# Kernel tuning notes

Hardware: AMD Instinct MI355X
Metric: run time of the kernel (lower is better)

The kernel has to match this reference:

```python
import jax, jax.numpy as jnp
import numpy as np

EPS = 1e-5

def _conv(x, w, groups=1):
    # x: NCHW, w: OIHW, VALID padding, stride 1
    return jax.lax.conv_general_dilated(
        x, w, window_strides=(1, 1), padding='VALID',
        feature_group_count=groups,
        dimension_numbers=('NCHW', 'OIHW', 'NCHW'))

def _bn(x, gamma, beta, mean, var):
    # eval-mode BatchNorm2d over channel dim
    inv = jax.lax.rsqrt(var + EPS) * gamma
    return x * inv[None, :, None, None] + (beta - mean * inv)[None, :, None, None]

def _xcorr_depthwise(x, kernel):
    # per-sample depthwise cross-correlation via grouped conv
    B, C, H, W = x.shape
    xr = x.reshape(1, B * C, H, W)
    kr = kernel.reshape(B * C, 1, kernel.shape[2], kernel.shape[3])
    out = _conv(xr, kr, groups=B * C)  # [1, B*C, Ho, Wo]
    return out.reshape(B, C, out.shape[2], out.shape[3])

def setup_inputs() -> dict:
    key = jax.random.key(0)
    ks = jax.random.split(key, 16)
    B, Cin, H, Oc = 128, 256, 256, 256
    inp = {
        'kernel': jax.random.normal(ks[0], (B, Cin, 7, 7), jnp.float32),
        'search': jax.random.normal(ks[1], (B, Cin, 31, 31), jnp.float32),
        # conv_kernel tower
        'wk': jax.random.normal(ks[2], (H, Cin, 3, 3), jnp.float32) * 0.05,
        'gk': jax.random.normal(ks[3], (H,), jnp.float32) * 0.1 + 1.0,
        'bk': jax.random.normal(ks[4], (H,), jnp.float32) * 0.1,
        'mk': jax.random.normal(ks[5], (H,), jnp.float32) * 0.1,
        'vk': jax.random.uniform(ks[6], (H,), jnp.float32) + 0.5,
        # conv_search tower
        'ws': jax.random.normal(ks[7], (H, Cin, 3, 3), jnp.float32) * 0.05,
        'gs': jax.random.normal(ks[8], (H,), jnp.float32) * 0.1 + 1.0,
        'bs': jax.random.normal(ks[9], (H,), jnp.float32) * 0.1,
        'ms': jax.random.normal(ks[10], (H,), jnp.float32) * 0.1,
        'vs': jax.random.uniform(ks[11], (H,), jnp.float32) + 0.5,
        # head: 1x1 conv -> BN -> ReLU -> 1x1 conv (with bias)
        'wh1': jax.random.normal(ks[12], (H, H, 1, 1), jnp.float32) * 0.05,
        'gh': jax.random.normal(ks[13], (H,), jnp.float32) * 0.1 + 1.0,
        'bh': jax.random.normal(ks[14], (H,), jnp.float32) * 0.1,
        'mh': jnp.zeros((H,), jnp.float32),
        'vh': jnp.ones((H,), jnp.float32),
        'wh2': jax.random.normal(ks[15], (Oc, H, 1, 1), jnp.float32) * 0.05,
        'bh2': jnp.zeros((Oc,), jnp.float32),
    }
    return inp

def reference(kernel, search, wk, gk, bk, mk, vk, ws, gs, bs, ms, vs,
              wh1, gh, bh, mh, vh, wh2, bh2):
    k = jax.nn.relu(_bn(_conv(kernel, wk), gk, bk, mk, vk))   # [B,H,5,5]
    s = jax.nn.relu(_bn(_conv(search, ws), gs, bs, ms, vs))   # [B,H,29,29]
    feat = _xcorr_depthwise(s, k)                              # [B,H,25,25]
    h = jax.nn.relu(_bn(_conv(feat, wh1), gh, bh, mh, vh))
    out = _conv(h, wh2) + bh2[None, :, None, None]            # [B,Oc,25,25]
    return out
```

## Files before the change

### kernel.cpp

```cpp
#include <hip/hip_runtime.h>
#include <hip/hip_bf16.h>
#include <cstdint>
#include <cstddef>

typedef unsigned short u16;
typedef __attribute__((ext_vector_type(8))) __bf16 bf16x8;
typedef __attribute__((ext_vector_type(4))) float f32x4;

#define EPS_BN 1e-5f

__device__ __forceinline__ u16 f2bf(float f) {
    union { float f; uint32_t u; } v; v.f = f;
    uint32_t u = v.u;
    u += 0x7FFFu + ((u >> 16) & 1u);
    return (u16)(u >> 16);
}
__device__ __forceinline__ float bf2f(u16 s) {
    union { uint32_t u; float f; } v; v.u = ((uint32_t)s) << 16;
    return v.f;
}

union Pack8 { u16 u[8]; uint4 v4; };
union Pack4 { u16 u[4]; uint2 v2; };

typedef __attribute__((address_space(1))) const unsigned char as1c;
typedef __attribute__((address_space(3))) unsigned char as3;
__device__ __forceinline__ void gld_lds16(const void* g, void* l) {
    __builtin_amdgcn_global_load_lds((as1c*)g, (as3*)l, 16, 0, 0);
}

__device__ __forceinline__ void tr_tile(const float* __restrict__ in,
                                        u16* __restrict__ out,
                                        int P, int b, int p0)
{
    const int cp = threadIdx.x & 31;
    const int pr = threadIdx.x >> 5;
    const float* ib = in + (size_t)b * 256 * P + (size_t)cp * 8 * P;
    u16* ob = out + (size_t)(b * P + p0) * 256 + cp * 8;

    #pragma unroll
    for (int it = 0; it < 8; it++) {
        int px = it * 8 + pr;
        int p  = p0 + px;
        bool ok = (p < P);
        int pc = ok ? p : (P - 1);
        Pack8 pk;
        #pragma unroll
        for (int i = 0; i < 8; i++)
            pk.u[i] = f2bf(ib[(size_t)i * P + pc]);
        if (ok) *(uint4*)(ob + (size_t)px * 256) = pk.v4;
    }
}

__global__ __launch_bounds__(256)
void tr_all(const float* __restrict__ s, const float* __restrict__ k,
            u16* __restrict__ so, u16* __restrict__ ko)
{
    int blk = blockIdx.x;
    if (blk < 2048) {
        tr_tile(s, so, 961, blk >> 4, (blk & 15) * 64);
    } else {
        tr_tile(k, ko, 49, blk - 2048, 0);
    }
}

template<int TAPS, bool NHWC_OUT, typename OutT, bool RELU>
__global__ __launch_bounds__(256)
void conv_gemm(const u16* __restrict__ in, const u16* __restrict__ W,
               const float* __restrict__ scale, const float* __restrict__ shift,
               OutT* __restrict__ out, int Hi, int Wi, int Ho, int Wo)
{
    constexpr int KT = TAPS * 256;
    constexpr int KB = KT / 64;
    const int HoWo = Ho * Wo;

    __shared__ u16 Alds[8192];
    __shared__ u16 Blds[8192];

    const int tid = threadIdx.x;
    const int it = blockIdx.x;
    const int jt = blockIdx.y;
    const int wv = tid >> 6;
    const int lane = tid & 63;

    const int c8 = tid & 7;
    const int t3 = tid >> 3;
    const int csw = c8 ^ (t3 & 7);

    const u16* gA[4];
    const u16* gB[4];
    #pragma unroll
    for (int q = 0; q < 4; q++) {
        int r = q * 32 + t3;
        gA[q] = W + (size_t)(it * 128 + r) * KT + csw * 8;
        int jg = jt * 128 + r;
        int bb = jg / HoWo;
        int msp = jg - bb * HoWo;
        int oyp = msp / Wo;
        int oxp = msp - oyp * Wo;
        gB[q] = in + ((size_t)(bb * Hi + oyp) * Wi + oxp) * 256 + csw * 8;
    }

    const int wi = (wv >> 1) * 64;
    const int wj = (wv & 1) * 64;
    const int lr = lane & 15;
    const int lq = lane >> 4;

    f32x4 acc[4][4];
    #pragma unroll
    for (int a = 0; a < 4; a++)
        #pragma unroll
        for (int b = 0; b < 4; b++)
            acc[a][b] = (f32x4){0.f, 0.f, 0.f, 0.f};

    for (int kb = 0; kb < KB; kb++) {
        const int tap = (TAPS == 1) ? 0 : (kb >> 2);
        const int c0  = (TAPS == 1) ? (kb * 64) : ((kb & 3) * 64);
        int ky = 0, kx = 0;
        if (TAPS == 9) { ky = tap / 3; kx = tap - ky * 3; }
        const int aoff = tap * 256 + c0;
        const int boff = (ky * Wi + kx) * 256 + c0;
        __syncthreads();
        #pragma unroll
        for (int q = 0; q < 4; q++)
            gld_lds16(gA[q] + aoff, Alds + q * 2048 + wv * 512);
        #pragma unroll
        for (int q = 0; q < 4; q++)
            gld_lds16(gB[q] + boff, Blds + q * 2048 + wv * 512);
        __syncthreads();
        #pragma unroll
        for (int ks = 0; ks < 2; ks++) {
            bf16x8 af[4], bfr[4];
            const int ck = ks * 4 + lq;
            #pragma unroll
            for (int f = 0; f < 4; f++) {
                int ra = wi + f * 16 + lr;
                af[f]  = *(const bf16x8*)&Alds[ra * 64 + ((ck ^ (ra & 7)) * 8)];
                int rb = wj + f * 16 + lr;
                bfr[f] = *(const bf16x8*)&Blds[rb * 64 + ((ck ^ (rb & 7)) * 8)];
            }
            #pragma unroll
            for (int fi = 0; fi < 4; fi++)
                #pragma unroll
                for (int fj = 0; fj < 4; fj++)
                    acc[fi][fj] = __builtin_amdgcn_mfma_f32_16x16x32_bf16(
                        af[fi], bfr[fj], acc[fi][fj], 0, 0, 0);
        }
    }

    if constexpr (NHWC_OUT) {
        int jc[4];
        #pragma unroll
        for (int fj = 0; fj < 4; fj++) jc[fj] = jt * 128 + wj + fj * 16 + lr;
        #pragma unroll
        for (int fi = 0; fi < 4; fi++) {
            int rb = it * 128 + wi + fi * 16 + lq * 4;
            f32x4 sc = *(const f32x4*)&scale[rb];
            f32x4 sh = *(const f32x4*)&shift[rb];
            #pragma unroll
            for (int fj = 0; fj < 4; fj++) {
                Pack4 pk;
                #pragma unroll
                for (int reg = 0; reg < 4; reg++) {
                    float v = acc[fi][fj][reg] * sc[reg] + sh[reg];
                    if (RELU) v = fmaxf(v, 0.f);
                    pk.u[reg] = f2bf(v);
                }
                *(uint2*)&((u16*)out)[(size_t)jc[fj] * 256 + rb] = pk.v2;
            }
        }
    } else {
        int jcb[4], jcm[4];
        #pragma unroll
        for (int fj = 0; fj < 4; fj++) {
            int jc = jt * 128 + wj + fj * 16 + lr;
            int b = jc / HoWo;
            jcb[fj] = b; jcm[fj] = jc - b * HoWo;
        }
        #pragma unroll
        for (int fi = 0; fi < 4; fi++) {
            int rb = it * 128 + wi + fi * 16 + lq * 4;
            f32x4 sc = *(const f32x4*)&scale[rb];
            f32x4 sh = *(const f32x4*)&shift[rb];
            #pragma unroll
            for (int reg = 0; reg < 4; reg++) {
                int r = rb + reg;
                #pragma unroll
                for (int fj = 0; fj < 4; fj++) {
                    float v = acc[fi][fj][reg] * sc[reg] + sh[reg];
                    if (RELU) v = fmaxf(v, 0.f);
                    size_t o = ((size_t)(jcb[fj] * 256 + r)) * HoWo + jcm[fj];
                    ((float*)out)[o] = v;
                }
            }
        }
    }
}

template<int TAPS>
__global__ __launch_bounds__(512, 2)
void conv_gemm8(const u16* __restrict__ in, const u16* __restrict__ W,
                const float* __restrict__ scale, const float* __restrict__ shift,
                u16* __restrict__ out, int Hi, int Wi, int Ho, int Wo, int npix)
{
    constexpr int KT = TAPS * 256;
    constexpr int NT = KT / 64;
    static_assert(NT >= 2, "pipeline needs >=2 K-tiles");
    const int HoWo = Ho * Wo;

    __shared__ u16 ldsbuf[65536];

    const int tid  = threadIdx.x;
    const int jt   = blockIdx.x;
    const int wv   = tid >> 6;
    const int lane = tid & 63;
    const int wm   = wv >> 2;
    const int wn   = wv & 3;
    const int lr   = lane & 15;
    const int lq   = lane >> 4;

    const int c8  = tid & 7;
    const int rr  = tid >> 3;
    const int csw = (c8 ^ (rr & 7)) * 8;

    const u16* gA00 = W + (size_t)(rr)        * KT + csw;
    const u16* gA01 = W + (size_t)(64  + rr)  * KT + csw;
    const u16* gA10 = W + (size_t)(128 + rr)  * KT + csw;
    const u16* gA11 = W + (size_t)(192 + rr)  * KT + csw;

    const u16* gB00; const u16* gB01; const u16* gB10; const u16* gB11;
    {
        #pragma unroll
        for (int hq = 0; hq < 4; hq++) {
            int jg = jt * 256 + hq * 64 + rr;
            if (jg >= npix) jg = npix - 1;
            int bb  = jg / HoWo;
            int msp = jg - bb * HoWo;
            int oy  = msp / Wo;
            int ox  = msp - oy * Wo;
            const u16* p = in + ((size_t)((bb * Hi + oy) * Wi + ox)) * 256 + csw;
            if (hq == 0) gB00 = p; else if (hq == 1) gB01 = p;
            else if (hq == 2) gB10 = p; else gB11 = p;
        }
    }

    #define STA(slot_, h_, j_) do { if ((j_) < NT) {                          \
        const int _ao = (j_) * 64;                                            \
        u16* _d = ldsbuf + (slot_) * 32768 + (h_) * 8192 + wv * 512;          \
        gld_lds16(((h_) ? gA10 : gA00) + _ao, _d);                            \
        gld_lds16(((h_) ? gA11 : gA01) + _ao, _d + 4096);                     \
    } } while (0)

    #define STB(slot_, h_, j_) do { if ((j_) < NT) {                          \
        int _ky = 0, _kx = 0;                                                 \
        if (TAPS == 9) { int _t = (j_) >> 2; _ky = _t / 3; _kx = _t - _ky*3; }\
        const int _bo = (_ky * Wi + _kx) * 256 + ((j_) & 3) * 64;             \
        u16* _d = ldsbuf + (slot_) * 32768 + 16384 + (h_) * 8192 + wv * 512;  \
        gld_lds16(((h_) ? gB10 : gB00) + _bo, _d);                            \
        gld_lds16(((h_) ? gB11 : gB01) + _bo, _d + 4096);                     \
    } } while (0)

    #define DSA(RQ) do {                                                      \
        _Pragma("unroll")                                                     \
        for (int ks = 0; ks < 2; ks++) {                                      \
            const int _cx = ks ? x1 : x0;                                     \
            _Pragma("unroll")                                                 \
            for (int f = 0; f < 4; f++) {                                     \
                int _ra = wm * 128 + (RQ) * 64 + f * 16 + lr;                 \
                aF[ks][f] = *(const bf16x8*)&ldsbuf[sA + _ra * 64 + _cx];     \
            }                                                                 \
        }                                                                     \
    } while (0)

    #define DSB(BF, CQ) do {                                                  \
        _Pragma("unroll")                                                     \
        for (int ks = 0; ks < 2; ks++) {                                      \
            const int _cx = ks ? x1 : x0;                                     \
            _Pragma("unroll")                                                 \
            for (int g = 0; g < 2; g++) {                                     \
                int _rb = wn * 64 + (CQ) * 32 + g * 16 + lr;                  \
                BF[ks][g] = *(const bf16x8*)&ldsbuf[sB + _rb * 64 + _cx];     \
            }                                                                 \
        }                                                                     \
    } while (0)

    #define MFMA16(AF, BF, RO, CO) do {                                       \
        __builtin_amdgcn_s_setprio(1);                                        \
        _Pragma("unroll")                                                     \
        for (int ks = 0; ks < 2; ks++)                                        \
            _Pragma("unroll")                                                 \
            for (int f = 0; f < 4; f++)                                       \
                _Pragma("unroll")                                             \
                for (int g = 0; g < 2; g++)                                   \
                    acc[(RO) + f][(CO) + g] =                                 \
                        __builtin_amdgcn_mfma_f32_16x16x32_bf16(              \
                            AF[ks][f], BF[ks][g], acc[(RO) + f][(CO) + g],    \
                            0, 0, 0);                                         \
        __builtin_amdgcn_s_setprio(0);                                        \
    } while (0)

    f32x4 acc[8][4];
    #pragma unroll
    for (int a = 0; a < 8; a++)
        #pragma unroll
        for (int b = 0; b < 4; b++)
            acc[a][b] = (f32x4){0.f, 0.f, 0.f, 0.f};

    const int x0 = ((0 * 4 + lq) ^ (lr & 7)) * 8;
    const int x1 = ((1 * 4 + lq) ^ (lr & 7)) * 8;

    STA(0, 0, 0); STA(0, 1, 0); STB(0, 0, 0); STB(0, 1, 0);
    STB(1, 0, 1); STA(1, 0, 1);
    asm volatile("s_waitcnt vmcnt(4)" ::: "memory");
    __builtin_amdgcn_s_barrier();

    for (int j = 0; j < NT; j++) {
        const int slot = j & 1;
        const int nsl  = slot ^ 1;
        const int sA   = slot * 32768;
        const int sB   = sA + 16384;
        bf16x8 aF[2][4], bF0[2][2], bF1[2][2];

        DSA(0); DSB(bF0, 0);
        STA(nsl, 1, j + 1);
        __builtin_amdgcn_s_barrier();
        asm volatile("s_waitcnt lgkmcnt(0)" ::: "memory");
        MFMA16(aF, bF0, 0, 0);
        __builtin_amdgcn_s_barrier();

        DSB(bF1, 1);
        STB(nsl, 1, j + 1);
        __builtin_amdgcn_s_barrier();
        asm volatile("s_waitcnt lgkmcnt(0)" ::: "memory");
        MFMA16(aF, bF1, 0, 2);
        __builtin_amdgcn_s_barrier();

        DSA(1);
        STB(slot, 0, j + 2);
        __builtin_amdgcn_s_barrier();
        asm volatile("s_waitcnt lgkmcnt(0)" ::: "memory");
        MFMA16(aF, bF0, 4, 0);
        __builtin_amdgcn_s_barrier();

        STA(slot, 0, j + 2);
        if (j + 2 < NT) asm volatile("s_waitcnt vmcnt(4)" ::: "memory");
        else            asm volatile("s_waitcnt vmcnt(0)" ::: "memory");
        __builtin_amdgcn_s_barrier();
        MFMA16(aF, bF1, 4, 2);
        __builtin_amdgcn_s_barrier();
    }

    #undef STA
    #undef STB
    #undef DSA
    #undef DSB
    #undef MFMA16

    const int obase = jt * 256;
    #pragma unroll
    for (int fr = 0; fr < 8; fr++) {
        const int rb = wm * 128 + fr * 16 + lq * 4;
        const f32x4 sc = *(const f32x4*)&scale[rb];
        const f32x4 sh = *(const f32x4*)&shift[rb];
        #pragma unroll
        for (int fc = 0; fc < 4; fc++) {
            const int jc = obase + wn * 64 + fc * 16 + lr;
            if (jc < npix) {
                Pack4 pk;
                #pragma unroll
                for (int reg = 0; reg < 4; reg++) {
                    float v = acc[fr][fc][reg] * sc[reg] + sh[reg];
                    v = fmaxf(v, 0.f);
                    pk.u[reg] = f2bf(v);
                }
                *(uint2*)&out[(size_t)jc * 256 + rb] = pk.v2;
            }
        }
    }
}

__global__ __launch_bounds__(256)
void xcorr_kernel(const u16* __restrict__ s, const u16* __restrict__ k,
                  u16* __restrict__ out)
{
    const int b = blockIdx.x / 25;
    const int oy = blockIdx.x - b * 25;
    const int c = threadIdx.x;

    float kf[25];
    #pragma unroll
    for (int t = 0; t < 25; t++)
        kf[t] = bf2f(k[((size_t)(b * 25 + t)) * 256 + c]);

    float acc[25];
    #pragma unroll
    for (int i = 0; i < 25; i++) acc[i] = 0.f;

    for (int dy = 0; dy < 5; dy++) {
        float row[29];
        const u16* sp = s + ((size_t)(b * 29 + oy + dy) * 29) * 256 + c;
        #pragma unroll
        for (int x = 0; x < 29; x++) row[x] = bf2f(sp[(size_t)x * 256]);
        #pragma unroll
        for (int dx = 0; dx < 5; dx++) {
            float kv = kf[dy * 5 + dx];
            #pragma unroll
            for (int ox = 0; ox < 25; ox++)
                acc[ox] += row[ox + dx] * kv;
        }
    }
    u16* op = out + ((size_t)(b * 25 + oy) * 25) * 256 + c;
    #pragma unroll
    for (int ox = 0; ox < 25; ox++)
        op[(size_t)ox * 256] = f2bf(acc[ox]);
}

__global__ __launch_bounds__(256)
void prep_all(const float* __restrict__ wk, const float* __restrict__ wsw,
              const float* __restrict__ wh1, const float* __restrict__ wh2,
              const float* gk, const float* bk, const float* mk, const float* vk,
              const float* gs, const float* bs, const float* ms, const float* vs,
              const float* gh, const float* bh, const float* mh, const float* vh,
              const float* bh2,
              u16* __restrict__ Wk2, u16* __restrict__ Ws2,
              u16* __restrict__ Wh1b, u16* __restrict__ Wh2b,
              float* sk, float* tk, float* ss, float* ts,
              float* sh, float* th, float* s5, float* t5)
{
    int blk = blockIdx.x;
    int tidx = threadIdx.x;
    if (blk < 4608) {
        const float* w = (blk < 2304) ? wk : wsw;
        u16* o = (blk < 2304) ? Wk2 : Ws2;
        int idx = (blk % 2304) * 256 + tidx;
        int oc = idx / 2304, rem = idx - oc * 2304;
        int tap = rem >> 8, c = rem & 255;
        o[idx] = f2bf(w[oc * 2304 + c * 9 + tap]);
    } else if (blk < 5120) {
        const float* w = (blk < 4864) ? wh1 : wh2;
        u16* o = (blk < 4864) ? Wh1b : Wh2b;
        int idx = ((blk - 4608) % 256) * 256 + tidx;
        o[idx] = f2bf(w[idx]);
    } else {
        int i = tidx;
        float iv;
        iv = rsqrtf(vk[i] + EPS_BN) * gk[i]; sk[i] = iv; tk[i] = bk[i] - mk[i] * iv;
        iv = rsqrtf(vs[i] + EPS_BN) * gs[i]; ss[i] = iv; ts[i] = bs[i] - ms[i] * iv;
        iv = rsqrtf(vh[i] + EPS_BN) * gh[i]; sh[i] = iv; th[i] = bh[i] - mh[i] * iv;
        s5[i] = 1.f; t5[i] = bh2[i];
    }
}

extern "C" void kernel_launch(void* const* d_in, const int* in_sizes, int n_in,
                              void* d_out, int out_size, void* d_ws, size_t ws_size,
                              hipStream_t stream)
{
    const float* in_kernel = (const float*)d_in[0];
    const float* in_search = (const float*)d_in[1];
    const float* wk  = (const float*)d_in[2];
    const float* gk  = (const float*)d_in[3];
    const float* bk  = (const float*)d_in[4];
    const float* mk  = (const float*)d_in[5];
    const float* vk  = (const float*)d_in[6];
    const float* wsw = (const float*)d_in[7];
    const float* gs  = (const float*)d_in[8];
    const float* bs  = (const float*)d_in[9];
    const float* ms  = (const float*)d_in[10];
    const float* vs  = (const float*)d_in[11];
    const float* wh1 = (const float*)d_in[12];
    const float* gh  = (const float*)d_in[13];
    const float* bh  = (const float*)d_in[14];
    const float* mh  = (const float*)d_in[15];
    const float* vh  = (const float*)d_in[16];
    const float* wh2 = (const float*)d_in[17];
    const float* bh2 = (const float*)d_in[18];
    float* out = (float*)d_out;

    char* w = (char*)d_ws;
    u16* Wk2 = (u16*)w;  w += 1179648;
    u16* Ws2 = (u16*)w;  w += 1179648;
    u16* Wh1 = (u16*)w;  w += 131072;
    u16* Wh2 = (u16*)w;  w += 131072;
    float* sk = (float*)w; w += 1024;
    float* tk = (float*)w; w += 1024;
    float* ss = (float*)w; w += 1024;
    float* ts = (float*)w; w += 1024;
    float* sh = (float*)w; w += 1024;
    float* th = (float*)w; w += 1024;
    float* s5 = (float*)w; w += 1024;
    float* t5 = (float*)w; w += 1024;
    u16* kfeat = (u16*)w; w += 1638400;
    u16* sfeat = (u16*)w; w += 55115776;
    u16* feat  = (u16*)w; w += 40960000;
    u16* ktr   = (u16*)w; w += 3211264;
    u16* strA  = (u16*)w; w += 62980096;
    u16* hbuf  = strA;

    tr_all<<<2048 + 128, 256, 0, stream>>>(in_search, in_kernel, strA, ktr);
    prep_all<<<5121, 256, 0, stream>>>(wk, wsw, wh1, wh2,
                                       gk, bk, mk, vk, gs, bs, ms, vs,
                                       gh, bh, mh, vh, bh2,
                                       Wk2, Ws2, Wh1, Wh2,
                                       sk, tk, ss, ts, sh, th, s5, t5);

    conv_gemm<9, true, u16, true><<<dim3(2, 25), 256, 0, stream>>>(
        ktr, Wk2, sk, tk, kfeat, 7, 7, 5, 5);
    conv_gemm8<9><<<dim3(421), 512, 0, stream>>>(
        strA, Ws2, ss, ts, sfeat, 31, 31, 29, 29, 128 * 841);
    xcorr_kernel<<<128 * 25, 256, 0, stream>>>(sfeat, kfeat, feat);
    conv_gemm<1, true, u16, true><<<dim3(2, 625), 256, 0, stream>>>(
        feat, Wh1, sh, th, hbuf, 25, 25, 25, 25);
    conv_gemm<1, false, float, false><<<dim3(2, 625), 256, 0, stream>>>(
        hbuf, Wh2, s5, t5, out, 25, 25, 25, 25);

    (void)in_sizes; (void)n_in; (void)out_size; (void)ws_size;
}
```

Before: 621.4 us.

## Restructure NCHW->NHWC transpose loads and remap GEMM blocks per XCD

The transpose kernel now has each lane own one pixel and load 64 channels strided by P. Consecutive lanes therefore read contiguous pixels, which coalesces the global reads. Each lane then writes 128 contiguous bytes of bf16 output. Separately, conv_gemm8 remaps blockIdx so that blocks dispatched round-robin to the same XCD process adjacent tiles, which should improve L2 reuse of shared input rows. The cost is higher register pressure from the 64-float array in the transpose.

```diff
diff --git a/kernel.cpp b/kernel.cpp
--- a/kernel.cpp
+++ b/kernel.cpp
@@ -33,22 +33,28 @@
                                         u16* __restrict__ out,
                                         int P, int b, int p0)
 {
-    const int cp = threadIdx.x & 31;
-    const int pr = threadIdx.x >> 5;
-    const float* ib = in + (size_t)b * 256 * P + (size_t)cp * 8 * P;
-    u16* ob = out + (size_t)(b * P + p0) * 256 + cp * 8;
-
-    #pragma unroll
-    for (int it = 0; it < 8; it++) {
-        int px = it * 8 + pr;
-        int p  = p0 + px;
-        bool ok = (p < P);
-        int pc = ok ? p : (P - 1);
-        Pack8 pk;
-        #pragma unroll
-        for (int i = 0; i < 8; i++)
-            pk.u[i] = f2bf(ib[(size_t)i * P + pc]);
-        if (ok) *(uint4*)(ob + (size_t)px * 256) = pk.v4;
+    const int w  = threadIdx.x >> 6;
+    const int ln = threadIdx.x & 63;
+    const int p  = p0 + ln;
+    const bool ok = (p < P);
+    const int pc = ok ? p : (P - 1);
+    const float* ib = in + ((size_t)b * 256 + w * 64) * P + pc;
+
+    float v[64];
+    #pragma unroll
+    for (int i = 0; i < 64; i++)
+        v[i] = ib[(size_t)i * P];
+
+    if (ok) {
+        u16* ob = out + ((size_t)(b * P + p)) * 256 + w * 64;
+        #pragma unroll
+        for (int k = 0; k < 8; k++) {
+            Pack8 pk;
+            #pragma unroll
+            for (int i = 0; i < 8; i++)
+                pk.u[i] = f2bf(v[k * 8 + i]);
+            *(uint4*)(ob + k * 8) = pk.v4;
+        }
     }
 }
 
@@ -211,7 +217,12 @@
     __shared__ u16 ldsbuf[65536];
 
     const int tid  = threadIdx.x;
-    const int jt   = blockIdx.x;
+    const int jt0  = blockIdx.x;
+    const int nwg  = gridDim.x;
+    const int q8   = nwg >> 3, r8 = nwg & 7;
+    const int xcd  = jt0 & 7, sidx = jt0 >> 3;
+    const int jt   = (xcd < r8 ? xcd * (q8 + 1)
+                               : r8 * (q8 + 1) + (xcd - r8) * q8) + sidx;
     const int wv   = tid >> 6;
     const int lane = tid & 63;
     const int wm   = wv >> 2;
```

After: 549.7 us. 11.5% less time.
